# Kernel optimization log

Measured on AMD Instinct MI355X. Metric: run time of the kernel, lower is better.

## Reference

```python
import jax, jax.numpy as jnp
import numpy as np
from jax import lax

B, C, H, W = 8192, 256, 5, 5
G = 8
SE_HID = 64        # max(8, 256 // 4)
GN_EPS = 1e-5
MM_EPS = 1e-8


def group_norm(x, gamma, beta):
    # x: [B, C, H, W]; normalize per (group, H, W)
    b = x.shape[0]
    xg = x.reshape(b, G, C // G, H, W)
    mean = xg.mean(axis=(2, 3, 4), keepdims=True)
    var = xg.var(axis=(2, 3, 4), keepdims=True)
    xg = (xg - mean) * lax.rsqrt(var + GN_EPS)
    xn = xg.reshape(b, C, H, W)
    return xn * gamma[None, :, None, None] + beta[None, :, None, None]


def setup_inputs() -> dict:
    key = jax.random.key(0)
    ks = jax.random.split(key, 10)
    x = jax.random.normal(ks[0], (B, C, H, W), dtype=jnp.float32)
    pair_mask = (jax.random.uniform(ks[1], (B, 1, H, W)) < 0.8).astype(jnp.float32)
    s1 = 1.0 / np.sqrt(C)
    W1 = jax.random.normal(ks[2], (C, C), dtype=jnp.float32) * s1          # 1x1 conv
    W2 = jax.random.normal(ks[3], (C, C, 3, 3), dtype=jnp.float32) * (s1 / 3.0)
    g1 = jnp.ones((C,), jnp.float32); b1 = jnp.zeros((C,), jnp.float32)
    g2 = jnp.ones((C,), jnp.float32); b2 = jnp.zeros((C,), jnp.float32)
    fc1_w = jax.random.normal(ks[4], (SE_HID, C), dtype=jnp.float32) * s1
    fc1_b = jnp.zeros((SE_HID,), jnp.float32)
    fc2_w = jax.random.normal(ks[5], (C, SE_HID), dtype=jnp.float32) / np.sqrt(SE_HID)
    fc2_b = jnp.zeros((C,), jnp.float32)
    return {"x": x, "pair_mask": pair_mask, "W1": W1, "g1": g1, "b1": b1,
            "W2": W2, "g2": g2, "b2": b2,
            "fc1_w": fc1_w, "fc1_b": fc1_b, "fc2_w": fc2_w, "fc2_b": fc2_b}


def reference(x, pair_mask, W1, g1, b1, W2, g2, b2, fc1_w, fc1_b, fc2_w, fc2_b):
    residual = x
    # conv1: 1x1, no bias -> channel mixing
    out = jnp.einsum('bchw,oc->bohw', x, W1)
    out = jax.nn.gelu(group_norm(out, g1, b1), approximate=False)
    # conv2: 3x3, padding=1, no bias
    out = lax.conv_general_dilated(out, W2, window_strides=(1, 1),
                                   padding=((1, 1), (1, 1)),
                                   dimension_numbers=('NCHW', 'OIHW', 'NCHW'))
    out = jax.nn.gelu(group_norm(out, g2, b2), approximate=False)
    out = out + residual
    # masked SE
    denom = jnp.maximum(pair_mask.sum(axis=(-1, -2)), MM_EPS)   # [B,1]
    pooled = (out * pair_mask).sum(axis=(-1, -2)) / denom       # [B,C]
    h = jax.nn.gelu(pooled @ fc1_w.T + fc1_b, approximate=False)
    gate = jax.nn.sigmoid(h @ fc2_w.T + fc2_b)                  # [B,C]
    out = out * gate[:, :, None, None] * pair_mask              # SE mask
    out = out * pair_mask                                       # final mask
    return out, gate
```

## Files before the change

kernel.cpp:

```cpp
#include <hip/hip_runtime.h>
#include <math.h>


typedef short v8s  __attribute__((ext_vector_type(8)));
typedef short v4s  __attribute__((ext_vector_type(4)));
typedef float v16f __attribute__((ext_vector_type(16)));
typedef float v4f  __attribute__((ext_vector_type(4)));

#define NTHREADS 512
#define NB 2
#define CPB 528
#define YROWS 26
#define YSB (YROWS*CPB)

#define Y_BYTES  (NB*YSB)
#define GB_OFF   (Y_BYTES)
#define MASK_OFF (GB_OFF + 4096)
#define POOL_OFF (MASK_OFF + 256)
#define H_OFF    (POOL_OFF + 2048)
#define GATE_OFF (H_OFF + 512)
#define INVD_OFF (GATE_OFF + 2048)
#define SMEM_BYTES (INVD_OFF + 64)

__device__ __forceinline__ unsigned short f2bf(float f){
  unsigned u = __float_as_uint(f);
  u = u + 0x7fffu + ((u >> 16) & 1u);
  return (unsigned short)(u >> 16);
}
__device__ __forceinline__ float bf2f(unsigned short u){
  return __uint_as_float(((unsigned)u) << 16);
}
__device__ __forceinline__ float gelu_f(float v){
  float z  = fabsf(v) * 0.70710678118654752f;
  float t  = __builtin_amdgcn_rcpf(fmaf(0.3275911f, z, 1.0f));
  float e  = __builtin_amdgcn_exp2f(-z*z*1.4426950408889634f);
  float p  = fmaf(1.061405429f, t, -1.453152027f);
  p = fmaf(p, t, 1.421413741f);
  p = fmaf(p, t, -0.284496736f);
  p = fmaf(p, t, 0.254829592f);
  float er = fmaf(-p*t, e, 1.0f);
  er = __builtin_copysignf(er, v);
  return 0.5f*v*(1.0f + er);
}

__global__ void prep_kernel(const float* __restrict__ W1, const float* __restrict__ W2,
                            const float* __restrict__ fc1w, const float* __restrict__ fc2w,
                            unsigned short* __restrict__ w1p, unsigned short* __restrict__ w2p,
                            float* __restrict__ fc1t, float* __restrict__ fc2t)
{
  int t = blockIdx.x*blockDim.x + threadIdx.x;
  int stride = gridDim.x*blockDim.x;
  for (int i=t; i<16*256*16; i+=stride){
    int s=i>>12, o=(i>>4)&255, kk=i&15;
    w1p[i] = f2bf(W1[o*256 + s*16 + kk]);
  }
  for (int i=t; i<144*256*16; i+=stride){
    int s=i>>12, o=(i>>4)&255, kk=i&15;
    int tap=s>>4, u=s&15;
    w2p[i] = f2bf(W2[o*2304 + (u*16+kk)*9 + tap]);
  }
  for (int i=t; i<256*64; i+=stride){ int c=i>>6, h=i&63; fc1t[i]=fc1w[h*256+c]; }
  for (int i=t; i<64*256; i+=stride){ int k=i>>8, c=i&255; fc2t[i]=fc2w[c*64+k]; }
}

__global__ __launch_bounds__(NTHREADS, 6) void lrb_main(
    const float* __restrict__ xg, const float* __restrict__ maskg,
    const float* __restrict__ g1, const float* __restrict__ b1,
    const float* __restrict__ g2, const float* __restrict__ b2,
    const unsigned short* __restrict__ w1p, const unsigned short* __restrict__ w2p,
    const float* __restrict__ fc1t, const float* __restrict__ fc1b,
    const float* __restrict__ fc2t, const float* __restrict__ fc2b,
    float* __restrict__ outg, float* __restrict__ gateg)
{
  extern __shared__ char smem[];
  unsigned short* OUTFu = (unsigned short*)smem;
  float* GB   = (float*)(smem + GB_OFF);
  float* MS   = (float*)(smem + MASK_OFF);
  float* POOL = (float*)(smem + POOL_OFF);
  float* HS   = (float*)(smem + H_OFF);
  float* GT   = (float*)(smem + GATE_OFF);
  float* INVD = (float*)(smem + INVD_OFF);

  const int tid  = threadIdx.x;
  const int lane = tid & 63;
  const int wid  = tid >> 6;
  const int p    = lane & 31;
  const int half = lane >> 5;
  const int hx   = half << 4;
  const bool pv  = (p < 25);
  const int b0   = blockIdx.x * NB;

  {
    int4 z4; z4.x=z4.y=z4.z=z4.w=0;
    if (tid < 2*33){
      int nt = tid/33, cc = tid - nt*33;
      *(int4*)(smem + nt*YSB + 25*CPB + cc*16) = z4;
    }
    if (tid >= 64 && tid < 320){
      int c = tid - 64;
      GB[c]=g1[c]; GB[256+c]=b1[c]; GB[512+c]=g2[c]; GB[768+c]=b2[c];
    }
    if (tid >= 320 && tid < 320 + NB*32){
      int t2 = tid - 320;
      int nbb = t2>>5, pp = t2&31;
      MS[t2] = (pp < 25) ? maskg[(size_t)(b0+nbb)*25 + pp] : 0.f;
    }
  }

  const int pr = p/5, ps = p - 5*(p/5);
  const int aoff = (wid*32 + p)*32 + hx;
  const char* w1a = (const char*)w1p + aoff;
  const char* w2a = (const char*)w2p + aoff;
  const int prow1 = pv ? p : 25;
  const char* b1base[2] = { smem + prow1*CPB + hx, smem + YSB + prow1*CPB + hx };

  int roA[9];
  #pragma unroll
  for (int t=0; t<9; ++t){
    int dr = t/3, ds = t - 3*(t/3);
    bool v = pv && (pr+dr >= 1) && (pr+dr <= 5) && (ps+ds >= 1) && (ps+ds <= 5);
    int row = v ? (p + (dr-1)*5 + (ds-1)) : 25;
    roA[t] = row*CPB + hx;
  }

  v8s A1[2], B1[2][2];
  A1[0] = *(const v8s*)(w1a);
  A1[1] = *(const v8s*)(w1a + 8192);

  for (int i = tid; i < NB*25*32; i += NTHREADS){
    int nbb = i / 800;
    int rem = i - nbb*800;
    int pp  = rem >> 5;
    int c8  = rem & 31;
    const float* src = xg + ((size_t)(b0+nbb)*256 + c8*8)*25 + pp;
    v8s pk;
    #pragma unroll
    for (int k=0;k<8;++k) pk[k] = (short)f2bf(src[k*25]);
    *(v8s*)(smem + nbb*YSB + pp*CPB + c8*16) = pk;
  }
  __syncthreads();

  if (tid < NB){
    float s=0.f;
    #pragma unroll
    for (int pp=0;pp<25;++pp) s += MS[tid*32+pp];
    INVD[tid] = __builtin_amdgcn_rcpf(fmaxf(s, 1e-8f));
  }

  v16f acc1_0, acc1_1;
  #pragma unroll
  for (int j=0;j<16;++j){ acc1_0[j]=0.f; acc1_1[j]=0.f; }
  #pragma unroll
  for (int s0=0; s0<2; ++s0){
    B1[s0][0] = *(const v8s*)(b1base[0] + s0*32);
    B1[s0][1] = *(const v8s*)(b1base[1] + s0*32);
  }
  #pragma unroll
  for (int s=0; s<16; ++s){
    __builtin_amdgcn_s_setprio(1);
    acc1_0 = __builtin_amdgcn_mfma_f32_32x32x16_bf16(A1[s&1], B1[s&1][0], acc1_0, 0,0,0);
    acc1_1 = __builtin_amdgcn_mfma_f32_32x32x16_bf16(A1[s&1], B1[s&1][1], acc1_1, 0,0,0);
    __builtin_amdgcn_s_setprio(0);
    if (s+2 < 16){
      A1[s&1] = *(const v8s*)(w1a + (s+2)*8192);
      B1[s&1][0] = *(const v8s*)(b1base[0] + (s+2)*32);
      B1[s&1][1] = *(const v8s*)(b1base[1] + (s+2)*32);
    }
  }

  v8s A2[2], B2[2][2];
  A2[0] = *(const v8s*)(w2a);
  A2[1] = *(const v8s*)(w2a + 8192);

  {
    float s0a=0.f,q0a=0.f,s1a=0.f,q1a=0.f;
    #pragma unroll
    for (int j=0;j<16;++j){
      float v0 = acc1_0[j], v1 = acc1_1[j];
      s0a+=v0; q0a+=v0*v0; s1a+=v1; q1a+=v1*v1;
    }
    #pragma unroll
    for (int off=1; off<64; off<<=1){
      s0a += __shfl_xor(s0a, off, 64); q0a += __shfl_xor(q0a, off, 64);
      s1a += __shfl_xor(s1a, off, 64); q1a += __shfl_xor(q1a, off, 64);
    }
    __syncthreads();

    float mu0 = s0a*(1.f/800.f), mu1 = s1a*(1.f/800.f);
    float rstd0 = rsqrtf(q0a*(1.f/800.f) - mu0*mu0 + 1e-5f);
    float rstd1 = rsqrtf(q1a*(1.f/800.f) - mu1*mu1 + 1e-5f);
    if (pv){
      #pragma unroll
      for (int nt=0; nt<2; ++nt){
        float mu = nt ? mu1 : mu0, rstd = nt ? rstd1 : rstd0;
        char* dst = smem + nt*YSB + p*CPB + wid*64 + half*8;
        #pragma unroll
        for (int q=0;q<4;++q){
          v4s pk;
          #pragma unroll
          for (int i2=0;i2<4;++i2){
            int ch = wid*32 + q*8 + half*4 + i2;
            float v = nt ? acc1_1[4*q+i2] : acc1_0[4*q+i2];
            float f = (v-mu)*rstd*GB[ch]+GB[256+ch];
            pk[i2] = (short)f2bf(gelu_f(f));
          }
          *(v4s*)(dst + q*16) = pk;
        }
      }
    }
  }
  __syncthreads();

  v16f acc2_0, acc2_1;
  #pragma unroll
  for (int j=0;j<16;++j){ acc2_0[j]=0.f; acc2_1[j]=0.f; }

  #pragma unroll
  for (int s0=0; s0<2; ++s0){
    B2[s0][0] = *(const v8s*)(smem + roA[0] + s0*32);
    B2[s0][1] = *(const v8s*)(smem + YSB + roA[0] + s0*32);
  }
  #pragma unroll
  for (int s=0; s<144; ++s){
    __builtin_amdgcn_s_setprio(1);
    acc2_0 = __builtin_amdgcn_mfma_f32_32x32x16_bf16(A2[s&1], B2[s&1][0], acc2_0, 0,0,0);
    acc2_1 = __builtin_amdgcn_mfma_f32_32x32x16_bf16(A2[s&1], B2[s&1][1], acc2_1, 0,0,0);
    __builtin_amdgcn_s_setprio(0);
    if (s+2 < 144){
      int s2 = s+2;
      A2[s&1] = *(const v8s*)(w2a + s2*8192);
      int ro = roA[s2>>4];
      int co = (s2&15)*32;
      B2[s&1][0] = *(const v8s*)(smem + ro + co);
      B2[s&1][1] = *(const v8s*)(smem + YSB + ro + co);
    }
  }

  {
    float s0a=0.f,q0a=0.f,s1a=0.f,q1a=0.f;
    #pragma unroll
    for (int j=0;j<16;++j){
      float v0=acc2_0[j], v1=acc2_1[j];
      s0a+=v0; q0a+=v0*v0; s1a+=v1; q1a+=v1*v1;
    }
    #pragma unroll
    for (int off=1; off<64; off<<=1){
      s0a += __shfl_xor(s0a, off, 64); q0a += __shfl_xor(q0a, off, 64);
      s1a += __shfl_xor(s1a, off, 64); q1a += __shfl_xor(q1a, off, 64);
    }
    __syncthreads();

    float mu0 = s0a*(1.f/800.f), mu1 = s1a*(1.f/800.f);
    float rstd0 = rsqrtf(q0a*(1.f/800.f) - mu0*mu0 + 1e-5f);
    float rstd1 = rsqrtf(q1a*(1.f/800.f) - mu1*mu1 + 1e-5f);
    if (pv){
      const float* xr0 = xg + ((size_t)(b0+0)*256 + wid*32)*25 + p;
      const float* xr1 = xg + ((size_t)(b0+1)*256 + wid*32)*25 + p;
      #pragma unroll 4
      for (int j=0;j<16;++j){
        int crow = (j&3) + 8*(j>>2) + 4*half;
        int ch   = wid*32 + crow;
        float f0 = (acc2_0[j]-mu0)*rstd0*GB[512+ch]+GB[768+ch];
        f0 = gelu_f(f0) + xr0[crow*25];
        OUTFu[ch*25 + p] = f2bf(f0);
        float f1 = (acc2_1[j]-mu1)*rstd1*GB[512+ch]+GB[768+ch];
        f1 = gelu_f(f1) + xr1[crow*25];
        OUTFu[6400 + ch*25 + p] = f2bf(f1);
      }
    }
  }
  __syncthreads();

  {
    int nbb = tid >> 8, ch = tid & 255;
    const unsigned short* of = OUTFu + nbb*6400 + ch*25;
    const float* ms = MS + nbb*32;
    float dot = 0.f;
    #pragma unroll
    for (int pp=0; pp<25; ++pp) dot = fmaf(bf2f(of[pp]), ms[pp], dot);
    POOL[nbb*256 + ch] = dot;
  }
  __syncthreads();

  {
    int nbb  = tid >> 8;
    int hid  = (tid >> 2) & 63;
    int part = tid & 3;
    const float* pl = POOL + nbb*256 + part*64;
    const float* wp = fc1t + part*64*64 + hid;
    float dot = 0.f;
    #pragma unroll 8
    for (int c=0;c<64;++c) dot += wp[c*64]*pl[c];
    dot += __shfl_xor(dot, 1, 64);
    dot += __shfl_xor(dot, 2, 64);
    if (part == 0)
      HS[nbb*64+hid] = gelu_f(fmaf(INVD[nbb], dot, fc1b[hid]));
  }
  __syncthreads();
  {
    int ch = tid & 255, nbb = tid >> 8;
    const float* hp = HS + nbb*64;
    float dot = 0.f;
    #pragma unroll 8
    for (int k=0;k<64;++k) dot += fc2t[k*256+ch]*hp[k];
    dot += fc2b[ch];
    float gv = __builtin_amdgcn_rcpf(1.0f + __builtin_amdgcn_exp2f(-dot*1.4426950408889634f));
    GT[nbb*256+ch] = gv;
    gateg[(size_t)(b0+nbb)*256+ch] = gv;
  }
  __syncthreads();

  for (int i = tid; i < NB*800; i += NTHREADS){
    int nbb = (i >= 800);
    int r   = i - nbb*800;
    int e0  = r*8;
    v8s pk = *(const v8s*)(OUTFu + nbb*6400 + e0);
    float o[8];
    #pragma unroll
    for (int k=0;k<8;++k){
      int e = e0+k;
      int ch = e/25;
      int pp = e - ch*25;
      o[k] = bf2f((unsigned short)pk[k]) * GT[nbb*256+ch] * MS[nbb*32+pp];
    }
    float* dst = outg + (size_t)(b0+nbb)*6400 + e0;
    v4f a, b;
    a[0]=o[0]; a[1]=o[1]; a[2]=o[2]; a[3]=o[3];
    b[0]=o[4]; b[1]=o[5]; b[2]=o[6]; b[3]=o[7];
    *(v4f*)(dst)   = a;
    *(v4f*)(dst+4) = b;
  }
}

extern "C" void kernel_launch(void* const* d_in, const int* in_sizes, int n_in,
                              void* d_out, int out_size, void* d_ws, size_t ws_size,
                              hipStream_t stream)
{
  const float* xg   = (const float*)d_in[0];
  const float* pm   = (const float*)d_in[1];
  const float* W1   = (const float*)d_in[2];
  const float* g1   = (const float*)d_in[3];
  const float* b1   = (const float*)d_in[4];
  const float* W2   = (const float*)d_in[5];
  const float* g2   = (const float*)d_in[6];
  const float* b2   = (const float*)d_in[7];
  const float* fc1w = (const float*)d_in[8];
  const float* fc1b = (const float*)d_in[9];
  const float* fc2w = (const float*)d_in[10];
  const float* fc2b = (const float*)d_in[11];

  float* outg  = (float*)d_out;
  float* gateg = outg + (size_t)8192*256*25;

  unsigned short* w1p = (unsigned short*)d_ws;
  unsigned short* w2p = w1p + 16*256*16;
  float* fc1t = (float*)(w2p + 144*256*16);
  float* fc2t = fc1t + 256*64;

  prep_kernel<<<dim3(512), dim3(256), 0, stream>>>(W1, W2, fc1w, fc2w, w1p, w2p, fc1t, fc2t);

  hipFuncSetAttribute(reinterpret_cast<const void*>(lrb_main),
                      hipFuncAttributeMaxDynamicSharedMemorySize, (int)SMEM_BYTES);
  lrb_main<<<dim3(4096), dim3(NTHREADS), SMEM_BYTES, stream>>>(
      xg, pm, g1, b1, g2, b2, w1p, w2p, fc1t, fc1b, fc2t, fc2b, outg, gateg);
}
```

Baseline: 548.5 us.

## Remap waves to 64 channels x one sample to share B operand across MFMAs

Each wave now covers 64 output channels for a single sample instead of 32 channels for both samples. One LDS-loaded B fragment then feeds two MFMAs, while two weight A fragments come from global memory. This halves LDS reads per MFMA and doubles global weight fragment loads, and B gets a three-deep register prefetch ring. GroupNorm statistics still come from a per-wave reduction, which stays valid because each wave's 64 channels form two whole groups of one sample.

Result: slower. 624.1 us (+13.8%).

```diff
diff --git a/kernel.cpp b/kernel.cpp
--- a/kernel.cpp
+++ b/kernel.cpp
@@ -84,6 +84,8 @@
   const int tid  = threadIdx.x;
   const int lane = tid & 63;
   const int wid  = tid >> 6;
+  const int sn   = wid & 1;
+  const int mh   = wid >> 1;
   const int p    = lane & 31;
   const int half = lane >> 5;
   const int hx   = half << 4;
@@ -108,11 +110,12 @@
   }
 
   const int pr = p/5, ps = p - 5*(p/5);
-  const int aoff = (wid*32 + p)*32 + hx;
+  const int aoff = (mh*64 + p)*32 + hx;
   const char* w1a = (const char*)w1p + aoff;
   const char* w2a = (const char*)w2p + aoff;
   const int prow1 = pv ? p : 25;
-  const char* b1base[2] = { smem + prow1*CPB + hx, smem + YSB + prow1*CPB + hx };
+  const char* ybase = smem + sn*YSB;
+  const char* b1base = ybase + prow1*CPB + hx;
 
   int roA[9];
   #pragma unroll
@@ -123,9 +126,12 @@
     roA[t] = row*CPB + hx;
   }
 
-  v8s A1[2], B1[2][2];
-  A1[0] = *(const v8s*)(w1a);
-  A1[1] = *(const v8s*)(w1a + 8192);
+  v8s A1[2][2], B1b[3];
+  #pragma unroll
+  for (int s0=0; s0<2; ++s0){
+    A1[s0][0] = *(const v8s*)(w1a + s0*8192);
+    A1[s0][1] = *(const v8s*)(w1a + s0*8192 + 1024);
+  }
 
   for (int i = tid; i < NB*25*32; i += NTHREADS){
     int nbb = i / 800;
@@ -151,26 +157,26 @@
   #pragma unroll
   for (int j=0;j<16;++j){ acc1_0[j]=0.f; acc1_1[j]=0.f; }
   #pragma unroll
-  for (int s0=0; s0<2; ++s0){
-    B1[s0][0] = *(const v8s*)(b1base[0] + s0*32);
-    B1[s0][1] = *(const v8s*)(b1base[1] + s0*32);
-  }
+  for (int s0=0; s0<3; ++s0) B1b[s0] = *(const v8s*)(b1base + s0*32);
   #pragma unroll
   for (int s=0; s<16; ++s){
     __builtin_amdgcn_s_setprio(1);
-    acc1_0 = __builtin_amdgcn_mfma_f32_32x32x16_bf16(A1[s&1], B1[s&1][0], acc1_0, 0,0,0);
-    acc1_1 = __builtin_amdgcn_mfma_f32_32x32x16_bf16(A1[s&1], B1[s&1][1], acc1_1, 0,0,0);
+    acc1_0 = __builtin_amdgcn_mfma_f32_32x32x16_bf16(A1[s&1][0], B1b[s%3], acc1_0, 0,0,0);
+    acc1_1 = __builtin_amdgcn_mfma_f32_32x32x16_bf16(A1[s&1][1], B1b[s%3], acc1_1, 0,0,0);
     __builtin_amdgcn_s_setprio(0);
     if (s+2 < 16){
-      A1[s&1] = *(const v8s*)(w1a + (s+2)*8192);
-      B1[s&1][0] = *(const v8s*)(b1base[0] + (s+2)*32);
-      B1[s&1][1] = *(const v8s*)(b1base[1] + (s+2)*32);
-    }
-  }
-
-  v8s A2[2], B2[2][2];
-  A2[0] = *(const v8s*)(w2a);
-  A2[1] = *(const v8s*)(w2a + 8192);
+      A1[s&1][0] = *(const v8s*)(w1a + (s+2)*8192);
+      A1[s&1][1] = *(const v8s*)(w1a + (s+2)*8192 + 1024);
+    }
+    if (s+3 < 16) B1b[s%3] = *(const v8s*)(b1base + (s+3)*32);
+  }
+
+  v8s A2[2][2], B2b[3];
+  #pragma unroll
+  for (int s0=0; s0<2; ++s0){
+    A2[s0][0] = *(const v8s*)(w2a + s0*8192);
+    A2[s0][1] = *(const v8s*)(w2a + s0*8192 + 1024);
+  }
 
   {
     float s0a=0.f,q0a=0.f,s1a=0.f,q1a=0.f;
@@ -190,22 +196,21 @@
     float rstd0 = rsqrtf(q0a*(1.f/800.f) - mu0*mu0 + 1e-5f);
     float rstd1 = rsqrtf(q1a*(1.f/800.f) - mu1*mu1 + 1e-5f);
     if (pv){
+      char* dst = smem + sn*YSB + p*CPB + mh*128 + half*8;
       #pragma unroll
-      for (int nt=0; nt<2; ++nt){
-        float mu = nt ? mu1 : mu0, rstd = nt ? rstd1 : rstd0;
-        char* dst = smem + nt*YSB + p*CPB + wid*64 + half*8;
+      for (int q=0;q<4;++q){
+        v4s pk0, pk1;
         #pragma unroll
-        for (int q=0;q<4;++q){
-          v4s pk;
-          #pragma unroll
-          for (int i2=0;i2<4;++i2){
-            int ch = wid*32 + q*8 + half*4 + i2;
-            float v = nt ? acc1_1[4*q+i2] : acc1_0[4*q+i2];
-            float f = (v-mu)*rstd*GB[ch]+GB[256+ch];
-            pk[i2] = (short)f2bf(gelu_f(f));
-          }
-          *(v4s*)(dst + q*16) = pk;
+        for (int i2=0;i2<4;++i2){
+          int ch0 = mh*64 + q*8 + half*4 + i2;
+          float f0 = (acc1_0[4*q+i2]-mu0)*rstd0*GB[ch0]+GB[256+ch0];
+          pk0[i2] = (short)f2bf(gelu_f(f0));
+          int ch1 = ch0 + 32;
+          float f1 = (acc1_1[4*q+i2]-mu1)*rstd1*GB[ch1]+GB[256+ch1];
+          pk1[i2] = (short)f2bf(gelu_f(f1));
         }
+        *(v4s*)(dst + q*16)      = pk0;
+        *(v4s*)(dst + 64 + q*16) = pk1;
       }
     }
   }
@@ -216,23 +221,22 @@
   for (int j=0;j<16;++j){ acc2_0[j]=0.f; acc2_1[j]=0.f; }
 
   #pragma unroll
-  for (int s0=0; s0<2; ++s0){
-    B2[s0][0] = *(const v8s*)(smem + roA[0] + s0*32);
-    B2[s0][1] = *(const v8s*)(smem + YSB + roA[0] + s0*32);
-  }
+  for (int s0=0; s0<3; ++s0)
+    B2b[s0] = *(const v8s*)(ybase + roA[0] + s0*32);
+
   #pragma unroll
   for (int s=0; s<144; ++s){
     __builtin_amdgcn_s_setprio(1);
-    acc2_0 = __builtin_amdgcn_mfma_f32_32x32x16_bf16(A2[s&1], B2[s&1][0], acc2_0, 0,0,0);
-    acc2_1 = __builtin_amdgcn_mfma_f32_32x32x16_bf16(A2[s&1], B2[s&1][1], acc2_1, 0,0,0);
+    acc2_0 = __builtin_amdgcn_mfma_f32_32x32x16_bf16(A2[s&1][0], B2b[s%3], acc2_0, 0,0,0);
+    acc2_1 = __builtin_amdgcn_mfma_f32_32x32x16_bf16(A2[s&1][1], B2b[s%3], acc2_1, 0,0,0);
     __builtin_amdgcn_s_setprio(0);
     if (s+2 < 144){
-      int s2 = s+2;
-      A2[s&1] = *(const v8s*)(w2a + s2*8192);
-      int ro = roA[s2>>4];
-      int co = (s2&15)*32;
-      B2[s&1][0] = *(const v8s*)(smem + ro + co);
-      B2[s&1][1] = *(const v8s*)(smem + YSB + ro + co);
+      A2[s&1][0] = *(const v8s*)(w2a + (s+2)*8192);
+      A2[s&1][1] = *(const v8s*)(w2a + (s+2)*8192 + 1024);
+    }
+    if (s+3 < 144){
+      int s3 = s+3;
+      B2b[s%3] = *(const v8s*)(ybase + roA[s3>>4] + (s3&15)*32);
     }
   }
 
@@ -254,18 +258,19 @@
     float rstd0 = rsqrtf(q0a*(1.f/800.f) - mu0*mu0 + 1e-5f);
     float rstd1 = rsqrtf(q1a*(1.f/800.f) - mu1*mu1 + 1e-5f);
     if (pv){
-      const float* xr0 = xg + ((size_t)(b0+0)*256 + wid*32)*25 + p;
-      const float* xr1 = xg + ((size_t)(b0+1)*256 + wid*32)*25 + p;
+      const float* xr = xg + ((size_t)(b0+sn)*256 + mh*64)*25 + p;
+      unsigned short* of = OUTFu + sn*6400 + mh*64*25 + p;
       #pragma unroll 4
       for (int j=0;j<16;++j){
         int crow = (j&3) + 8*(j>>2) + 4*half;
-        int ch   = wid*32 + crow;
-        float f0 = (acc2_0[j]-mu0)*rstd0*GB[512+ch]+GB[768+ch];
-        f0 = gelu_f(f0) + xr0[crow*25];
-        OUTFu[ch*25 + p] = f2bf(f0);
-        float f1 = (acc2_1[j]-mu1)*rstd1*GB[512+ch]+GB[768+ch];
-        f1 = gelu_f(f1) + xr1[crow*25];
-        OUTFu[6400 + ch*25 + p] = f2bf(f1);
+        int ch0  = mh*64 + crow;
+        float f0 = (acc2_0[j]-mu0)*rstd0*GB[512+ch0]+GB[768+ch0];
+        f0 = gelu_f(f0) + xr[crow*25];
+        of[crow*25] = f2bf(f0);
+        int ch1  = ch0 + 32;
+        float f1 = (acc2_1[j]-mu1)*rstd1*GB[512+ch1]+GB[768+ch1];
+        f1 = gelu_f(f1) + xr[(32+crow)*25];
+        of[(32+crow)*25] = f2bf(f1);
       }
     }
   }
```

## Defer residual add to final store and pool residual during input staging

Applied to the files above, without the earlier changes.

The residual x is no longer added in the GN2 epilogue with strided scalar loads. It is re-read with coalesced vector loads in the final output loop and added there. Its masked-pool contribution is computed while staging x into LDS and accumulated into POOL with shared atomics, so pooling stays correct because pooling is linear. The conv2 weight prefetch distance is also raised from 2 to 4 stages. This adds an extra sync, LDS atomics and more registers, and x is now read twice from global memory (likely L2-resident). The residual is also no longer rounded into the bf16 buffer, which changes numerics slightly.

Measured after the change: 569.1 us. 1.04x slower.

```diff
diff --git a/kernel.cpp b/kernel.cpp
--- a/kernel.cpp
+++ b/kernel.cpp
@@ -105,7 +105,11 @@
       int nbb = t2>>5, pp = t2&31;
       MS[t2] = (pp < 25) ? maskg[(size_t)(b0+nbb)*25 + pp] : 0.f;
     }
-  }
+    if (tid >= 384 && tid < 384 + 128){
+      ((int4*)POOL)[tid-384] = z4;
+    }
+  }
+  __syncthreads();
 
   const int pr = p/5, ps = p - 5*(p/5);
   const int aoff = (wid*32 + p)*32 + hx;
@@ -127,16 +131,36 @@
   A1[0] = *(const v8s*)(w1a);
   A1[1] = *(const v8s*)(w1a + 8192);
 
-  for (int i = tid; i < NB*25*32; i += NTHREADS){
-    int nbb = i / 800;
-    int rem = i - nbb*800;
-    int pp  = rem >> 5;
+  {
+    int nbb = tid >> 8;
+    int rem = tid & 255;
+    int pg  = rem >> 5;
     int c8  = rem & 31;
-    const float* src = xg + ((size_t)(b0+nbb)*256 + c8*8)*25 + pp;
-    v8s pk;
-    #pragma unroll
-    for (int k=0;k<8;++k) pk[k] = (short)f2bf(src[k*25]);
-    *(v8s*)(smem + nbb*YSB + pp*CPB + c8*16) = pk;
+    int pp0 = pg*4;
+    float acc8[8];
+    #pragma unroll
+    for (int k=0;k<8;++k) acc8[k]=0.f;
+    const float* srcb = xg + ((size_t)(b0+nbb)*256 + c8*8)*25;
+    #pragma unroll
+    for (int j=0;j<4;++j){
+      int pp = pp0 + j;
+      if (pp < 25){
+        float mk = MS[nbb*32+pp];
+        v8s pk;
+        #pragma unroll
+        for (int k=0;k<8;++k){
+          float v = srcb[k*25 + pp];
+          pk[k] = (short)f2bf(v);
+          acc8[k] = fmaf(v, mk, acc8[k]);
+        }
+        *(v8s*)(smem + nbb*YSB + pp*CPB + c8*16) = pk;
+      }
+    }
+    if (pp0 < 25){
+      #pragma unroll
+      for (int k=0;k<8;++k)
+        atomicAdd(&POOL[nbb*256 + c8*8 + k], acc8[k]);
+    }
   }
   __syncthreads();
 
@@ -168,9 +192,9 @@
     }
   }
 
-  v8s A2[2], B2[2][2];
-  A2[0] = *(const v8s*)(w2a);
-  A2[1] = *(const v8s*)(w2a + 8192);
+  v8s A2[4], B2[2][2];
+  #pragma unroll
+  for (int s0=0; s0<4; ++s0) A2[s0] = *(const v8s*)(w2a + s0*8192);
 
   {
     float s0a=0.f,q0a=0.f,s1a=0.f,q1a=0.f;
@@ -223,12 +247,12 @@
   #pragma unroll
   for (int s=0; s<144; ++s){
     __builtin_amdgcn_s_setprio(1);
-    acc2_0 = __builtin_amdgcn_mfma_f32_32x32x16_bf16(A2[s&1], B2[s&1][0], acc2_0, 0,0,0);
-    acc2_1 = __builtin_amdgcn_mfma_f32_32x32x16_bf16(A2[s&1], B2[s&1][1], acc2_1, 0,0,0);
+    acc2_0 = __builtin_amdgcn_mfma_f32_32x32x16_bf16(A2[s&3], B2[s&1][0], acc2_0, 0,0,0);
+    acc2_1 = __builtin_amdgcn_mfma_f32_32x32x16_bf16(A2[s&3], B2[s&1][1], acc2_1, 0,0,0);
     __builtin_amdgcn_s_setprio(0);
+    if (s+4 < 144) A2[s&3] = *(const v8s*)(w2a + (s+4)*8192);
     if (s+2 < 144){
       int s2 = s+2;
-      A2[s&1] = *(const v8s*)(w2a + s2*8192);
       int ro = roA[s2>>4];
       int co = (s2&15)*32;
       B2[s&1][0] = *(const v8s*)(smem + ro + co);
@@ -254,18 +278,14 @@
     float rstd0 = rsqrtf(q0a*(1.f/800.f) - mu0*mu0 + 1e-5f);
     float rstd1 = rsqrtf(q1a*(1.f/800.f) - mu1*mu1 + 1e-5f);
     if (pv){
-      const float* xr0 = xg + ((size_t)(b0+0)*256 + wid*32)*25 + p;
-      const float* xr1 = xg + ((size_t)(b0+1)*256 + wid*32)*25 + p;
       #pragma unroll 4
       for (int j=0;j<16;++j){
         int crow = (j&3) + 8*(j>>2) + 4*half;
         int ch   = wid*32 + crow;
         float f0 = (acc2_0[j]-mu0)*rstd0*GB[512+ch]+GB[768+ch];
-        f0 = gelu_f(f0) + xr0[crow*25];
-        OUTFu[ch*25 + p] = f2bf(f0);
+        OUTFu[ch*25 + p] = f2bf(gelu_f(f0));
         float f1 = (acc2_1[j]-mu1)*rstd1*GB[512+ch]+GB[768+ch];
-        f1 = gelu_f(f1) + xr1[crow*25];
-        OUTFu[6400 + ch*25 + p] = f2bf(f1);
+        OUTFu[6400 + ch*25 + p] = f2bf(gelu_f(f1));
       }
     }
   }
@@ -275,7 +295,7 @@
     int nbb = tid >> 8, ch = tid & 255;
     const unsigned short* of = OUTFu + nbb*6400 + ch*25;
     const float* ms = MS + nbb*32;
-    float dot = 0.f;
+    float dot = POOL[nbb*256 + ch];
     #pragma unroll
     for (int pp=0; pp<25; ++pp) dot = fmaf(bf2f(of[pp]), ms[pp], dot);
     POOL[nbb*256 + ch] = dot;
@@ -315,13 +335,17 @@
     int r   = i - nbb*800;
     int e0  = r*8;
     v8s pk = *(const v8s*)(OUTFu + nbb*6400 + e0);
+    const float* xs = xg + (size_t)(b0+nbb)*6400 + e0;
+    v4f x0 = *(const v4f*)(xs);
+    v4f x1 = *(const v4f*)(xs + 4);
     float o[8];
     #pragma unroll
     for (int k=0;k<8;++k){
       int e = e0+k;
       int ch = e/25;
       int pp = e - ch*25;
-      o[k] = bf2f((unsigned short)pk[k]) * GT[nbb*256+ch] * MS[nbb*32+pp];
+      float xv = (k < 4) ? x0[k] : x1[k-4];
+      o[k] = (bf2f((unsigned short)pk[k]) + xv) * GT[nbb*256+ch] * MS[nbb*32+pp];
     }
     float* dst = outg + (size_t)(b0+nbb)*6400 + e0;
     v4f a, b;
```

## Split conv2 K across wave pairs with 2x2 MFMA tiles and LDS reduction

Applied to the files above, without the earlier changes.

Conv2 is restructured so each pair of waves covers 64 output channels and splits the K dimension in half. Each wave computes a 2x2 block of MFMA tiles, so every A and B fragment is reused twice and the per-wave loop shrinks from 144 to 72 steps. The partial sums are exchanged through LDS in bf16 and added, and each wave then finishes one sample. Occupancy is lowered to 4 waves per SIMD to leave room for the extra accumulators, setprio hints are removed, and the bf16 partial-sum exchange adds rounding error plus extra barriers.

After: 702.2 us. 28.0% more time.

```diff
diff --git a/kernel.cpp b/kernel.cpp
--- a/kernel.cpp
+++ b/kernel.cpp
@@ -43,6 +43,30 @@
   return 0.5f*v*(1.0f + er);
 }
 
+__device__ __forceinline__ void ex_store(char* base, int lane, const v16f &v){
+  int4 a, b;
+  unsigned* pa = (unsigned*)&a; unsigned* pb = (unsigned*)&b;
+  #pragma unroll
+  for (int i=0;i<4;++i){
+    pa[i] = (unsigned)f2bf(v[2*i])   | ((unsigned)f2bf(v[2*i+1])   << 16);
+    pb[i] = (unsigned)f2bf(v[8+2*i]) | ((unsigned)f2bf(v[8+2*i+1]) << 16);
+  }
+  *(int4*)(base + lane*16)        = a;
+  *(int4*)(base + 1024 + lane*16) = b;
+}
+__device__ __forceinline__ void ex_addload(const char* base, int lane, v16f &v){
+  int4 a = *(const int4*)(base + lane*16);
+  int4 b = *(const int4*)(base + 1024 + lane*16);
+  const unsigned* pa = (const unsigned*)&a; const unsigned* pb = (const unsigned*)&b;
+  #pragma unroll
+  for (int i=0;i<4;++i){
+    v[2*i]     += bf2f((unsigned short)(pa[i] & 0xffff));
+    v[2*i+1]   += bf2f((unsigned short)(pa[i] >> 16));
+    v[8+2*i]   += bf2f((unsigned short)(pb[i] & 0xffff));
+    v[8+2*i+1] += bf2f((unsigned short)(pb[i] >> 16));
+  }
+}
+
 __global__ void prep_kernel(const float* __restrict__ W1, const float* __restrict__ W2,
                             const float* __restrict__ fc1w, const float* __restrict__ fc2w,
                             unsigned short* __restrict__ w1p, unsigned short* __restrict__ w2p,
@@ -63,7 +87,7 @@
   for (int i=t; i<64*256; i+=stride){ int k=i>>8, c=i&255; fc2t[i]=fc2w[c*64+k]; }
 }
 
-__global__ __launch_bounds__(NTHREADS, 6) void lrb_main(
+__global__ __launch_bounds__(NTHREADS, 4) void lrb_main(
     const float* __restrict__ xg, const float* __restrict__ maskg,
     const float* __restrict__ g1, const float* __restrict__ b1,
     const float* __restrict__ g2, const float* __restrict__ b2,
@@ -84,6 +108,8 @@
   const int tid  = threadIdx.x;
   const int lane = tid & 63;
   const int wid  = tid >> 6;
+  const int mp   = wid >> 1;
+  const int kh   = wid & 1;
   const int p    = lane & 31;
   const int half = lane >> 5;
   const int hx   = half << 4;
@@ -108,11 +134,12 @@
   }
 
   const int pr = p/5, ps = p - 5*(p/5);
-  const int aoff = (wid*32 + p)*32 + hx;
-  const char* w1a = (const char*)w1p + aoff;
-  const char* w2a = (const char*)w2p + aoff;
+  const char* w1a = (const char*)w1p + (wid*32 + p)*32 + hx;
   const int prow1 = pv ? p : 25;
   const char* b1base[2] = { smem + prow1*CPB + hx, smem + YSB + prow1*CPB + hx };
+
+  const char* w2base = (const char*)w2p + kh*65536 + mp*2048 + p*32 + hx;
+  const int bcol = hx + kh*256;
 
   int roA[9];
   #pragma unroll
@@ -120,7 +147,7 @@
     int dr = t/3, ds = t - 3*(t/3);
     bool v = pv && (pr+dr >= 1) && (pr+dr <= 5) && (ps+ds >= 1) && (ps+ds <= 5);
     int row = v ? (p + (dr-1)*5 + (ds-1)) : 25;
-    roA[t] = row*CPB + hx;
+    roA[t] = row*CPB;
   }
 
   v8s A1[2], B1[2][2];
@@ -157,10 +184,8 @@
   }
   #pragma unroll
   for (int s=0; s<16; ++s){
-    __builtin_amdgcn_s_setprio(1);
     acc1_0 = __builtin_amdgcn_mfma_f32_32x32x16_bf16(A1[s&1], B1[s&1][0], acc1_0, 0,0,0);
     acc1_1 = __builtin_amdgcn_mfma_f32_32x32x16_bf16(A1[s&1], B1[s&1][1], acc1_1, 0,0,0);
-    __builtin_amdgcn_s_setprio(0);
     if (s+2 < 16){
       A1[s&1] = *(const v8s*)(w1a + (s+2)*8192);
       B1[s&1][0] = *(const v8s*)(b1base[0] + (s+2)*32);
@@ -168,9 +193,13 @@
     }
   }
 
-  v8s A2[2], B2[2][2];
-  A2[0] = *(const v8s*)(w2a);
-  A2[1] = *(const v8s*)(w2a + 8192);
+  v8s A2[3][2], B2[2][2];
+  #pragma unroll
+  for (int s0=0; s0<3; ++s0){
+    const char* ap = w2base + (s0>>3)*131072 + (s0&7)*8192;
+    A2[s0][0] = *(const v8s*)(ap);
+    A2[s0][1] = *(const v8s*)(ap + 1024);
+  }
 
   {
     float s0a=0.f,q0a=0.f,s1a=0.f,q1a=0.f;
@@ -211,36 +240,57 @@
   }
   __syncthreads();
 
-  v16f acc2_0, acc2_1;
-  #pragma unroll
-  for (int j=0;j<16;++j){ acc2_0[j]=0.f; acc2_1[j]=0.f; }
+  v16f acc2_00, acc2_01, acc2_10, acc2_11;
+  #pragma unroll
+  for (int j=0;j<16;++j){ acc2_00[j]=0.f; acc2_01[j]=0.f; acc2_10[j]=0.f; acc2_11[j]=0.f; }
 
   #pragma unroll
   for (int s0=0; s0<2; ++s0){
-    B2[s0][0] = *(const v8s*)(smem + roA[0] + s0*32);
-    B2[s0][1] = *(const v8s*)(smem + YSB + roA[0] + s0*32);
-  }
-  #pragma unroll
-  for (int s=0; s<144; ++s){
-    __builtin_amdgcn_s_setprio(1);
-    acc2_0 = __builtin_amdgcn_mfma_f32_32x32x16_bf16(A2[s&1], B2[s&1][0], acc2_0, 0,0,0);
-    acc2_1 = __builtin_amdgcn_mfma_f32_32x32x16_bf16(A2[s&1], B2[s&1][1], acc2_1, 0,0,0);
-    __builtin_amdgcn_s_setprio(0);
-    if (s+2 < 144){
+    B2[s0][0] = *(const v8s*)(smem + roA[0] + bcol + s0*32);
+    B2[s0][1] = *(const v8s*)(smem + YSB + roA[0] + bcol + s0*32);
+  }
+  #pragma unroll
+  for (int s=0; s<72; ++s){
+    acc2_00 = __builtin_amdgcn_mfma_f32_32x32x16_bf16(A2[s%3][0], B2[s&1][0], acc2_00, 0,0,0);
+    acc2_01 = __builtin_amdgcn_mfma_f32_32x32x16_bf16(A2[s%3][0], B2[s&1][1], acc2_01, 0,0,0);
+    acc2_10 = __builtin_amdgcn_mfma_f32_32x32x16_bf16(A2[s%3][1], B2[s&1][0], acc2_10, 0,0,0);
+    acc2_11 = __builtin_amdgcn_mfma_f32_32x32x16_bf16(A2[s%3][1], B2[s&1][1], acc2_11, 0,0,0);
+    if (s+3 < 72){
+      int s3 = s+3;
+      const char* ap = w2base + (s3>>3)*131072 + (s3&7)*8192;
+      A2[s%3][0] = *(const v8s*)(ap);
+      A2[s%3][1] = *(const v8s*)(ap + 1024);
+    }
+    if (s+2 < 72){
       int s2 = s+2;
-      A2[s&1] = *(const v8s*)(w2a + s2*8192);
-      int ro = roA[s2>>4];
-      int co = (s2&15)*32;
+      int ro = roA[s2>>3];
+      int co = bcol + (s2&7)*32;
       B2[s&1][0] = *(const v8s*)(smem + ro + co);
       B2[s&1][1] = *(const v8s*)(smem + YSB + ro + co);
     }
   }
+  __syncthreads();
+
+  {
+    char* EXw = smem + ((kh^1)*4 + mp)*2048;
+    const char* EXr = smem + (kh*4 + mp)*2048;
+    ex_store(EXw, lane, (kh==0) ? acc2_01 : acc2_00);
+    __syncthreads();
+    if (kh==0) ex_addload(EXr, lane, acc2_00); else ex_addload(EXr, lane, acc2_01);
+    __syncthreads();
+    ex_store(EXw, lane, (kh==0) ? acc2_11 : acc2_10);
+    __syncthreads();
+    if (kh==0) ex_addload(EXr, lane, acc2_10); else ex_addload(EXr, lane, acc2_11);
+    __syncthreads();
+  }
+  v16f F0 = (kh==0) ? acc2_00 : acc2_01;
+  v16f F1 = (kh==0) ? acc2_10 : acc2_11;
 
   {
     float s0a=0.f,q0a=0.f,s1a=0.f,q1a=0.f;
     #pragma unroll
     for (int j=0;j<16;++j){
-      float v0=acc2_0[j], v1=acc2_1[j];
+      float v0=F0[j], v1=F1[j];
       s0a+=v0; q0a+=v0*v0; s1a+=v1; q1a+=v1*v1;
     }
     #pragma unroll
@@ -248,24 +298,23 @@
       s0a += __shfl_xor(s0a, off, 64); q0a += __shfl_xor(q0a, off, 64);
       s1a += __shfl_xor(s1a, off, 64); q1a += __shfl_xor(q1a, off, 64);
     }
-    __syncthreads();
-
     float mu0 = s0a*(1.f/800.f), mu1 = s1a*(1.f/800.f);
     float rstd0 = rsqrtf(q0a*(1.f/800.f) - mu0*mu0 + 1e-5f);
     float rstd1 = rsqrtf(q1a*(1.f/800.f) - mu1*mu1 + 1e-5f);
     if (pv){
-      const float* xr0 = xg + ((size_t)(b0+0)*256 + wid*32)*25 + p;
-      const float* xr1 = xg + ((size_t)(b0+1)*256 + wid*32)*25 + p;
+      const float* xr = xg + ((size_t)(b0+kh)*256 + mp*64)*25 + p;
+      unsigned short* of = OUTFu + kh*6400 + mp*64*25 + p;
       #pragma unroll 4
       for (int j=0;j<16;++j){
         int crow = (j&3) + 8*(j>>2) + 4*half;
-        int ch   = wid*32 + crow;
-        float f0 = (acc2_0[j]-mu0)*rstd0*GB[512+ch]+GB[768+ch];
-        f0 = gelu_f(f0) + xr0[crow*25];
-        OUTFu[ch*25 + p] = f2bf(f0);
-        float f1 = (acc2_1[j]-mu1)*rstd1*GB[512+ch]+GB[768+ch];
-        f1 = gelu_f(f1) + xr1[crow*25];
-        OUTFu[6400 + ch*25 + p] = f2bf(f1);
+        int ch0  = mp*64 + crow;
+        float f0 = (F0[j]-mu0)*rstd0*GB[512+ch0]+GB[768+ch0];
+        f0 = gelu_f(f0) + xr[crow*25];
+        of[crow*25] = f2bf(f0);
+        int ch1  = ch0 + 32;
+        float f1 = (F1[j]-mu1)*rstd1*GB[512+ch1]+GB[768+ch1];
+        f1 = gelu_f(f1) + xr[(32+crow)*25];
+        of[(32+crow)*25] = f2bf(f1);
       }
     }
   }
```
